# Performance work log

Hardware: AMD Instinct MI355X
Metric: run time of the kernel (lower is better)

Reference implementation:

```python
import jax, jax.numpy as jnp
import numpy as np

B = 1024          # batch
H = 512           # hidden_dim
T = 256           # seq_len
CD = 2            # coord_dim
LAT = 64 + 64 + 128  # total latent dim


def setup_inputs() -> dict:
    key = jax.random.key(0)
    ks = jax.random.split(key, 20)
    s = 0.05  # weight init scale
    rn = lambda k, shp: (jax.random.normal(k, shp, dtype=jnp.float32) * s)
    return {
        "z_primitive": jax.random.normal(ks[0], (B, 64), dtype=jnp.float32),
        "z_skill": jax.random.normal(ks[1], (B, 64), dtype=jnp.float32),
        "z_style": jax.random.normal(ks[2], (B, 128), dtype=jnp.float32),
        "W_proj": rn(ks[3], (2 * H, LAT)),
        "b_proj": jnp.zeros((2 * H,), jnp.float32),
        "Wih1": rn(ks[4], (4 * H, CD)),
        "Whh1": rn(ks[5], (4 * H, H)),
        "bih1": jnp.zeros((4 * H,), jnp.float32),
        "bhh1": jnp.zeros((4 * H,), jnp.float32),
        "Wih2": rn(ks[6], (4 * H, H)),
        "Whh2": rn(ks[7], (4 * H, H)),
        "bih2": jnp.zeros((4 * H,), jnp.float32),
        "bhh2": jnp.zeros((4 * H,), jnp.float32),
        "Wo1": rn(ks[8], (H // 2, H)),
        "bo1": jnp.zeros((H // 2,), jnp.float32),
        "Wo2": rn(ks[9], (CD, H // 2)),
        "bo2": jnp.zeros((CD,), jnp.float32),
    }


def _lstm_cell(x, h, c, Wih, Whh, bih, bhh):
    # PyTorch gate order: i, f, g, o
    gates = x @ Wih.T + h @ Whh.T + (bih + bhh)
    i, f, g, o = jnp.split(gates, 4, axis=1)
    c_new = jax.nn.sigmoid(f) * c + jax.nn.sigmoid(i) * jnp.tanh(g)
    h_new = jax.nn.sigmoid(o) * jnp.tanh(c_new)
    return h_new, c_new


def reference(z_primitive, z_skill, z_style, W_proj, b_proj,
              Wih1, Whh1, bih1, bhh1, Wih2, Whh2, bih2, bhh2,
              Wo1, bo1, Wo2, bo2):
    z = jnp.concatenate([z_primitive, z_skill, z_style], axis=1)  # [B, LAT]
    init = z @ W_proj.T + b_proj                                  # [B, 2H]
    h0 = init[:, :H]
    c0 = init[:, H:]
    x0 = jnp.zeros((z.shape[0], CD), init.dtype)

    def step(carry, _):
        x, h1, c1, h2, c2 = carry
        h1, c1 = _lstm_cell(x, h1, c1, Wih1, Whh1, bih1, bhh1)
        h2, c2 = _lstm_cell(h1, h2, c2, Wih2, Whh2, bih2, bhh2)
        # output MLP (Dropout inactive in eval)
        y = jax.nn.relu(h2 @ Wo1.T + bo1) @ Wo2.T + bo2  # [B, CD]
        return (y, h1, c1, h2, c2), y

    # h0/c0 repeated across both LSTM layers (repeat(2,1,1) in torch)
    _, ys = jax.lax.scan(step, (x0, h0, c0, h0, c0), None, length=T)
    return jnp.transpose(ys, (1, 0, 2))  # [B, T, CD]
```

## Files before the change

kernel.cpp:

```cpp
#include <hip/hip_runtime.h>
#include <math.h>

#define NB 1024
#define NH 512
#define NT 256
#define NCD 2

typedef unsigned short u16;
typedef __bf16 bf16x8 __attribute__((ext_vector_type(8)));
typedef float  f32x4  __attribute__((ext_vector_type(4)));

#define MFMA_BF16 __builtin_amdgcn_mfma_f32_16x16x32_bf16

__device__ __forceinline__ float sigf(float x) { return 1.0f / (1.0f + expf(-x)); }
__device__ __forceinline__ float b2f(u16 u) {
    union { unsigned i; float f; } v; v.i = ((unsigned)u) << 16; return v.f;
}
__device__ __forceinline__ u16 f2b(float f) {
    union { float f; unsigned i; } v; v.f = f;
    unsigned r = v.i + 0x7fffu + ((v.i >> 16) & 1u);
    return (u16)(r >> 16);
}

__device__ __forceinline__ void async_cp16(const void* gptr, void* lptr) {
    __builtin_amdgcn_global_load_lds(
        (const __attribute__((address_space(1))) unsigned int*)gptr,
        (__attribute__((address_space(3))) unsigned int*)lptr,
        16, 0, 0);
}

__global__ __launch_bounds__(256) void convert3(
    const float* __restrict__ a, const float* __restrict__ b,
    const float* __restrict__ c,
    u16* __restrict__ oa, u16* __restrict__ ob, u16* __restrict__ oc)
{
    const int i = blockIdx.x * 256 + threadIdx.x;
    oa[i] = f2b(a[i]); ob[i] = f2b(b[i]); oc[i] = f2b(c[i]);
}

__global__ __launch_bounds__(256) void bsum_k(
    const float* __restrict__ bi1, const float* __restrict__ bh1,
    const float* __restrict__ bi2, const float* __restrict__ bh2,
    float* __restrict__ o1, float* __restrict__ o2)
{
    const int i = blockIdx.x * 256 + threadIdx.x;
    o1[i] = bi1[i] + bh1[i];
    o2[i] = bi2[i] + bh2[i];
}

__global__ __launch_bounds__(256) void transpose_wo1(
    const float* __restrict__ Wo1, u16* __restrict__ Wo1T)
{
    const int idx = blockIdx.x * 256 + threadIdx.x;
    const int r = idx >> 9, k = idx & 511;
    Wo1T[k * 256 + r] = f2b(Wo1[idx]);
}

__global__ __launch_bounds__(256) void init_kernel(
    const float* __restrict__ zp, const float* __restrict__ zs,
    const float* __restrict__ zst, const float* __restrict__ Wp,
    const float* __restrict__ bp,
    u16* __restrict__ h1, float* __restrict__ c1,
    u16* __restrict__ h2, float* __restrict__ c2)
{
    __shared__ float z[4][256];
    const int tid = threadIdx.x;
    const int b0  = blockIdx.x * 4;
    for (int i = tid; i < 4 * 256; i += 256) {
        const int bb = i >> 8, k = i & 255;
        float v;
        if (k < 64)       v = zp [(b0 + bb) * 64  + k];
        else if (k < 128) v = zs [(b0 + bb) * 64  + (k - 64)];
        else              v = zst[(b0 + bb) * 128 + (k - 128)];
        z[bb][k] = v;
    }
    __syncthreads();
    for (int rt = 0; rt < 4; ++rt) {
        const int r = rt * 256 + tid;
        const float bias = bp[r];
        float a0 = bias, a1 = bias, a2 = bias, a3 = bias;
        for (int k = 0; k < 256; ++k) {
            const float w = Wp[r * 256 + k];
            a0 += z[0][k] * w; a1 += z[1][k] * w;
            a2 += z[2][k] * w; a3 += z[3][k] * w;
        }
        const float acc[4] = {a0, a1, a2, a3};
        for (int bb = 0; bb < 4; ++bb) {
            const int b = b0 + bb;
            if (r < NH) {
                h1[b * NH + r] = f2b(acc[bb]);
                h2[b * NH + r] = f2b(acc[bb]);
            } else {
                c1[b * NH + r - NH] = acc[bb];
                c2[b * NH + r - NH] = acc[bb];
            }
        }
    }
}

__global__ __launch_bounds__(512, 4) void lstm_mfma32(
    const u16* __restrict__ A0, const u16* __restrict__ W0,
    const u16* __restrict__ A1, const u16* __restrict__ W1,
    const float* __restrict__ bsum,
    const float* __restrict__ xin, const float* __restrict__ Wx,
    float* __restrict__ c, u16* __restrict__ hnext,
    const int npass)
{
    __shared__ __align__(16) char smem[61440];
    float* eg = (float*)smem;

    const int tid  = threadIdx.x;
    const int lane = tid & 63;
    const int wv   = tid >> 6;
    const int g    = wv & 3;
    const int mh   = wv >> 2;
    const int l15  = lane & 15;
    const int q    = lane >> 4;
    const int bx   = blockIdx.x;
    const int ut   = (bx & 7) * 2 + ((bx >> 3) & 1);
    const int grp  = bx >> 4;
    const int b0   = grp * 32;
    const int u0   = ut * 32;

    int goffW0, goffW1, goffA = 0;
    {
        const int c0 = (wv * 2) * 64 + lane;
        const int w0r = c0 >> 3;
        goffW0 = ((w0r >> 5) * NH + u0 + (w0r & 31)) * NH + (((c0 & 7) ^ (w0r & 7)) * 8);
        const int c1i = (wv * 2 + 1) * 64 + lane;
        const int w1r = c1i >> 3;
        goffW1 = ((w1r >> 5) * NH + u0 + (w1r & 31)) * NH + (((c1i & 7) ^ (w1r & 7)) * 8);
        if (wv < 4) {
            const int ca = wv * 64 + lane;
            const int ar = ca >> 3;
            goffA = (b0 + ar) * NH + (((ca & 7) ^ (ar & 7)) * 8);
        }
    }

    f32x4 acc[2];
    acc[0] = (f32x4){0.f, 0.f, 0.f, 0.f};
    acc[1] = (f32x4){0.f, 0.f, 0.f, 0.f};

    const int M = npass * 8;

    auto issue = [&](int m, int bi) {
        const u16* __restrict__ Ap = (m < 8) ? A0 : A1;
        const u16* __restrict__ Wp = (m < 8) ? W0 : W1;
        const int k0 = (m & 7) * 64;
        char* base = smem + bi * 20480;
        async_cp16((const void*)(Wp + goffW0 + k0),
                   (void*)(base + 4096 + (wv * 2) * 1024));
        async_cp16((const void*)(Wp + goffW1 + k0),
                   (void*)(base + 4096 + (wv * 2 + 1) * 1024));
        if (wv < 4)
            async_cp16((const void*)(Ap + goffA + k0),
                       (void*)(base + wv * 1024));
    };

    issue(0, 0);
    if (M > 1) issue(1, 1);
    int ci = 0;
    for (int m = 0; m < M; ++m) {
        if (m + 1 < M) {
            if (wv < 4) asm volatile("s_waitcnt vmcnt(3)" ::: "memory");
            else        asm volatile("s_waitcnt vmcnt(2)" ::: "memory");
        } else {
            asm volatile("s_waitcnt vmcnt(0)" ::: "memory");
        }
        __builtin_amdgcn_s_barrier();
        if (m + 2 < M) {
            int bi = ci + 2; if (bi >= 3) bi -= 3;
            issue(m + 2, bi);
        }
        const char* bA = smem + ci * 20480;
        const char* bW = bA + 4096;
#pragma unroll
        for (int khi = 0; khi < 2; ++khi) {
            bf16x8 bfr[2];
#pragma unroll
            for (int ni = 0; ni < 2; ++ni) {
                const int wrow = g * 32 + ni * 16 + l15;
                const int j = (khi * 4 + q) ^ (wrow & 7);
                bfr[ni] = *(const bf16x8*)(bW + wrow * 128 + j * 16);
            }
            const int row = mh * 16 + l15;
            const int j = (khi * 4 + q) ^ (row & 7);
            const bf16x8 av = *(const bf16x8*)(bA + row * 128 + j * 16);
            acc[0] = MFMA_BF16(av, bfr[0], acc[0], 0, 0, 0);
            acc[1] = MFMA_BF16(av, bfr[1], acc[1], 0, 0, 0);
        }
        ++ci; if (ci == 3) ci = 0;
    }

    __syncthreads();
#pragma unroll
    for (int ni = 0; ni < 2; ++ni)
#pragma unroll
        for (int r = 0; r < 4; ++r)
            eg[(g * 32 + mh * 16 + q * 4 + r) * 33 + ni * 16 + l15] = acc[ni][r];
    __syncthreads();

    const int u  = tid & 31;
    const int bq = tid >> 5;
    const int ug = u0 + u;
    float bs[4], wx0[4], wx1[4];
#pragma unroll
    for (int g4 = 0; g4 < 4; ++g4) bs[g4] = bsum[g4 * NH + ug];
    if (Wx) {
#pragma unroll
        for (int g4 = 0; g4 < 4; ++g4) {
            wx0[g4] = Wx[(g4 * NH + ug) * 2 + 0];
            wx1[g4] = Wx[(g4 * NH + ug) * 2 + 1];
        }
    }
#pragma unroll
    for (int jj = 0; jj < 2; ++jj) {
        const int bl = bq * 2 + jj;
        const int b  = b0 + bl;
        float gv[4];
#pragma unroll
        for (int g4 = 0; g4 < 4; ++g4) gv[g4] = eg[(g4 * 32 + bl) * 33 + u] + bs[g4];
        if (Wx) {
            const float x0 = xin[b * 2], x1 = xin[b * 2 + 1];
#pragma unroll
            for (int g4 = 0; g4 < 4; ++g4) gv[g4] += x0 * wx0[g4] + x1 * wx1[g4];
        }
        const float iv = sigf(gv[0]);
        const float fv = sigf(gv[1]);
        const float gg = tanhf(gv[2]);
        const float ov = sigf(gv[3]);
        const size_t idx = (size_t)b * NH + ug;
        const float cn = fv * c[idx] + iv * gg;
        c[idx] = cn;
        hnext[idx] = f2b(ov * tanhf(cn));
    }
}

__global__ __launch_bounds__(256) void out_kernel(
    const u16* __restrict__ h2, const u16* __restrict__ W1t,
    const float* __restrict__ bo1, const float* __restrict__ Wo2,
    const float* __restrict__ bo2, float* __restrict__ xbuf,
    float* __restrict__ out, const int t)
{
    __shared__ float hsh[2 * NH];
    __shared__ float red[4][4];
    const int tid = threadIdx.x;
    const int b0  = blockIdx.x * 2;
    for (int i = tid; i < 2 * NH; i += 256)
        hsh[i] = b2f(h2[(size_t)b0 * NH + i]);
    __syncthreads();

    const int n = tid;
    float a0 = 0.f, a1 = 0.f;
#pragma unroll 16
    for (int k = 0; k < NH; ++k) {
        const float w = b2f(W1t[k * 256 + n]);
        a0 += hsh[k] * w;
        a1 += hsh[NH + k] * w;
    }
    const float bn = bo1[n], w20 = Wo2[n], w21 = Wo2[256 + n];
    const float s0 = fmaxf(a0 + bn, 0.f), s1 = fmaxf(a1 + bn, 0.f);
    float p[4] = { s0 * w20, s0 * w21, s1 * w20, s1 * w21 };
#pragma unroll
    for (int off = 32; off > 0; off >>= 1)
#pragma unroll
        for (int r = 0; r < 4; ++r) p[r] += __shfl_down(p[r], off, 64);
    const int wave = tid >> 6, lane = tid & 63;
    if (lane == 0)
#pragma unroll
        for (int r = 0; r < 4; ++r) red[r][wave] = p[r];
    __syncthreads();
    if (tid < 4) {
        const int rp = tid >> 1, cc = tid & 1;
        const float v = red[tid][0] + red[tid][1] + red[tid][2] + red[tid][3]
                        + bo2[cc];
        const int b = b0 + rp;
        xbuf[b * NCD + cc] = v;
        out[(size_t)b * (NT * NCD) + t * NCD + cc] = v;
    }
}

extern "C" void kernel_launch(void* const* d_in, const int* in_sizes, int n_in,
                              void* d_out, int out_size, void* d_ws, size_t ws_size,
                              hipStream_t stream)
{
    const float* zp   = (const float*)d_in[0];
    const float* zsk  = (const float*)d_in[1];
    const float* zst  = (const float*)d_in[2];
    const float* Wp   = (const float*)d_in[3];
    const float* bp   = (const float*)d_in[4];
    const float* Wih1 = (const float*)d_in[5];
    const float* Whh1 = (const float*)d_in[6];
    const float* bih1 = (const float*)d_in[7];
    const float* bhh1 = (const float*)d_in[8];
    const float* Wih2 = (const float*)d_in[9];
    const float* Whh2 = (const float*)d_in[10];
    const float* bih2 = (const float*)d_in[11];
    const float* bhh2 = (const float*)d_in[12];
    const float* Wo1  = (const float*)d_in[13];
    const float* bo1  = (const float*)d_in[14];
    const float* Wo2  = (const float*)d_in[15];
    const float* bo2  = (const float*)d_in[16];

    const size_t BH = (size_t)NB * NH;
    u16*   h1a   = (u16*)d_ws;
    u16*   h1b   = h1a + BH;
    u16*   h2a   = h1b + BH;
    u16*   h2b   = h2a + BH;
    float* c1    = (float*)(h2b + BH);
    float* c2    = c1 + BH;
    float* xb    = c2 + BH;
    float* bs1   = xb + 4096;
    float* bs2   = bs1 + 2048;
    u16*   Wo1T  = (u16*)(bs2 + 2048);
    u16*   Whh1b = Wo1T + 131072;
    u16*   Wih2b = Whh1b + 1048576;
    u16*   Whh2b = Wih2b + 1048576;

    convert3<<<(2048 * 512) / 256, 256, 0, stream>>>(Whh1, Wih2, Whh2, Whh1b, Wih2b, Whh2b);
    transpose_wo1<<<(256 * 512) / 256, 256, 0, stream>>>(Wo1, Wo1T);
    bsum_k<<<2048 / 256, 256, 0, stream>>>(bih1, bhh1, bih2, bhh2, bs1, bs2);
    hipMemsetAsync(xb, 0, NB * NCD * sizeof(float), stream);
    init_kernel<<<NB / 4, 256, 0, stream>>>(zp, zsk, zst, Wp, bp, h1a, c1, h2a, c2);

    u16* h1c = h1a; u16* h1n = h1b;
    u16* h2c = h2a; u16* h2n = h2b;
    float* outp = (float*)d_out;
    for (int t = 0; t < NT; ++t) {
        lstm_mfma32<<<512, 512, 0, stream>>>(h1c, Whh1b, (const u16*)0, (const u16*)0,
                                             bs1, xb, Wih1, c1, h1n, 1);
        lstm_mfma32<<<512, 512, 0, stream>>>(h1n, Wih2b, h2c, Whh2b,
                                             bs2, (const float*)0, (const float*)0, c2, h2n, 2);
        out_kernel<<<512, 256, 0, stream>>>(h2n, Wo1T, bo1, Wo2, bo2, xb, outp, t);
        u16* tmp = h1c; h1c = h1n; h1n = tmp;
        tmp = h2c; h2c = h2n; h2n = tmp;
    }
}
```

Baseline: 8.472 ms.

## Fuse output MLP into layer-1 LSTM kernel with inter-block flag synchronization

```diff
diff --git a/kernel.cpp b/kernel.cpp
--- a/kernel.cpp
+++ b/kernel.cpp
@@ -95,6 +95,200 @@
                 c2[b * NH + r - NH] = acc[bb];
             }
         }
+    }
+}
+
+__global__ __launch_bounds__(512, 4) void fused_out_lstm1(
+    const u16* __restrict__ h2prev,
+    const u16* __restrict__ A0,
+    const u16* __restrict__ W0,
+    const float* __restrict__ bsum,
+    float* __restrict__ xb,
+    const float* __restrict__ Wx,
+    const u16* __restrict__ W1t, const float* __restrict__ bo1,
+    const float* __restrict__ Wo2, const float* __restrict__ bo2,
+    float* __restrict__ outp,
+    float* __restrict__ c, u16* __restrict__ hnext,
+    unsigned* __restrict__ flags,
+    const int t, const int do_lstm)
+{
+    __shared__ __align__(16) char smem[61440];
+    float* eg = (float*)smem;
+
+    const int tid  = threadIdx.x;
+    const int lane = tid & 63;
+    const int wv   = tid >> 6;
+    const int g    = wv & 3;
+    const int mh   = wv >> 2;
+    const int l15  = lane & 15;
+    const int q    = lane >> 4;
+    const int bx   = blockIdx.x;
+    const int ut   = (bx & 7) * 2 + ((bx >> 3) & 1);
+    const int grp  = bx >> 4;
+    const int b0   = grp * 32;
+    const int u0   = ut * 32;
+    const int r0   = grp * 32 + ut * 2;
+
+    int goffW0, goffW1, goffA = 0;
+    {
+        const int c0 = (wv * 2) * 64 + lane;
+        const int w0r = c0 >> 3;
+        goffW0 = ((w0r >> 5) * NH + u0 + (w0r & 31)) * NH + (((c0 & 7) ^ (w0r & 7)) * 8);
+        const int c1i = (wv * 2 + 1) * 64 + lane;
+        const int w1r = c1i >> 3;
+        goffW1 = ((w1r >> 5) * NH + u0 + (w1r & 31)) * NH + (((c1i & 7) ^ (w1r & 7)) * 8);
+        if (wv < 4) {
+            const int ca = wv * 64 + lane;
+            const int ar = ca >> 3;
+            goffA = (b0 + ar) * NH + (((ca & 7) ^ (ar & 7)) * 8);
+        }
+    }
+
+    auto issue = [&](int m, int bi) {
+        const int k0 = (m & 7) * 64;
+        char* base = smem + bi * 20480;
+        async_cp16((const void*)(W0 + goffW0 + k0),
+                   (void*)(base + 4096 + (wv * 2) * 1024));
+        async_cp16((const void*)(W0 + goffW1 + k0),
+                   (void*)(base + 4096 + (wv * 2 + 1) * 1024));
+        if (wv < 4)
+            async_cp16((const void*)(A0 + goffA + k0),
+                       (void*)(base + wv * 1024));
+    };
+
+    if (do_lstm) { issue(0, 0); issue(1, 1); }
+
+    if (h2prev) {
+        float* hsh = (float*)(smem + 40960);
+        float* red = (float*)(smem + 40960 + 4096);
+        for (int i = tid; i < 2 * NH; i += 512)
+            hsh[i] = b2f(h2prev[(size_t)(r0 + (i >> 9)) * NH + (i & 511)]);
+        asm volatile("s_waitcnt lgkmcnt(0)" ::: "memory");
+        __builtin_amdgcn_s_barrier();
+        const int n  = tid & 255;
+        const int hh = tid >> 8;
+        const float* hr = hsh + hh * NH;
+        float a = 0.f;
+#pragma unroll 16
+        for (int k = 0; k < NH; ++k)
+            a += hr[k] * b2f(W1t[k * 256 + n]);
+        const float s = fmaxf(a + bo1[n], 0.f);
+        float p0 = s * Wo2[n], p1 = s * Wo2[256 + n];
+#pragma unroll
+        for (int off = 32; off > 0; off >>= 1) {
+            p0 += __shfl_down(p0, off, 64);
+            p1 += __shfl_down(p1, off, 64);
+        }
+        if (lane == 0) { red[wv * 2] = p0; red[wv * 2 + 1] = p1; }
+        asm volatile("s_waitcnt lgkmcnt(0)" ::: "memory");
+        __builtin_amdgcn_s_barrier();
+        if (tid < 4) {
+            const int hh2 = tid >> 1, cc = tid & 1;
+            const int wb = hh2 * 4;
+            const float y = red[wb * 2 + cc] + red[(wb + 1) * 2 + cc]
+                          + red[(wb + 2) * 2 + cc] + red[(wb + 3) * 2 + cc]
+                          + bo2[cc];
+            const int b = r0 + hh2;
+            xb[b * NCD + cc] = y;
+            outp[(size_t)b * (NT * NCD) + (t - 1) * NCD + cc] = y;
+        }
+        if (wv == 0) {
+            __builtin_amdgcn_fence(__ATOMIC_RELEASE, "agent");
+            if (lane == 0 && do_lstm)
+                __hip_atomic_store(&flags[(grp * 16 + ut) * 16], (unsigned)t,
+                                   __ATOMIC_RELAXED, __HIP_MEMORY_SCOPE_AGENT);
+        }
+    }
+    if (!do_lstm) return;
+
+    f32x4 acc[2];
+    acc[0] = (f32x4){0.f, 0.f, 0.f, 0.f};
+    acc[1] = (f32x4){0.f, 0.f, 0.f, 0.f};
+    const int M = 8;
+    int ci = 0;
+    for (int m = 0; m < M; ++m) {
+        if (m + 1 < M) {
+            if (wv < 4) asm volatile("s_waitcnt vmcnt(3)" ::: "memory");
+            else        asm volatile("s_waitcnt vmcnt(2)" ::: "memory");
+        } else {
+            asm volatile("s_waitcnt vmcnt(0)" ::: "memory");
+        }
+        __builtin_amdgcn_s_barrier();
+        if (m + 2 < M) {
+            int bi = ci + 2; if (bi >= 3) bi -= 3;
+            issue(m + 2, bi);
+        }
+        const char* bA = smem + ci * 20480;
+        const char* bW = bA + 4096;
+#pragma unroll
+        for (int khi = 0; khi < 2; ++khi) {
+            bf16x8 bfr[2];
+#pragma unroll
+            for (int ni = 0; ni < 2; ++ni) {
+                const int wrow = g * 32 + ni * 16 + l15;
+                const int j = (khi * 4 + q) ^ (wrow & 7);
+                bfr[ni] = *(const bf16x8*)(bW + wrow * 128 + j * 16);
+            }
+            const int row = mh * 16 + l15;
+            const int j = (khi * 4 + q) ^ (row & 7);
+            const bf16x8 av = *(const bf16x8*)(bA + row * 128 + j * 16);
+            acc[0] = MFMA_BF16(av, bfr[0], acc[0], 0, 0, 0);
+            acc[1] = MFMA_BF16(av, bfr[1], acc[1], 0, 0, 0);
+        }
+        ++ci; if (ci == 3) ci = 0;
+    }
+
+    __syncthreads();
+#pragma unroll
+    for (int ni = 0; ni < 2; ++ni)
+#pragma unroll
+        for (int r = 0; r < 4; ++r)
+            eg[(g * 32 + mh * 16 + q * 4 + r) * 33 + ni * 16 + l15] = acc[ni][r];
+    __syncthreads();
+
+    if (t > 0) {
+        if (tid < 16) {
+            const unsigned tu = (unsigned)t;
+            while (__hip_atomic_load(&flags[(grp * 16 + tid) * 16],
+                                     __ATOMIC_RELAXED,
+                                     __HIP_MEMORY_SCOPE_AGENT) < tu)
+                __builtin_amdgcn_s_sleep(2);
+        }
+        __syncthreads();
+    }
+
+    const int u  = tid & 31;
+    const int bq = tid >> 5;
+    const int ug = u0 + u;
+    float bs[4], wx0[4], wx1[4];
+#pragma unroll
+    for (int g4 = 0; g4 < 4; ++g4) bs[g4] = bsum[g4 * NH + ug];
+#pragma unroll
+    for (int g4 = 0; g4 < 4; ++g4) {
+        wx0[g4] = Wx[(g4 * NH + ug) * 2 + 0];
+        wx1[g4] = Wx[(g4 * NH + ug) * 2 + 1];
+    }
+#pragma unroll
+    for (int jj = 0; jj < 2; ++jj) {
+        const int bl = bq * 2 + jj;
+        const int b  = b0 + bl;
+        float gv[4];
+#pragma unroll
+        for (int g4 = 0; g4 < 4; ++g4) gv[g4] = eg[(g4 * 32 + bl) * 33 + u] + bs[g4];
+        const float x0 = __hip_atomic_load(&xb[b * 2 + 0], __ATOMIC_RELAXED,
+                                           __HIP_MEMORY_SCOPE_AGENT);
+        const float x1 = __hip_atomic_load(&xb[b * 2 + 1], __ATOMIC_RELAXED,
+                                           __HIP_MEMORY_SCOPE_AGENT);
+#pragma unroll
+        for (int g4 = 0; g4 < 4; ++g4) gv[g4] += x0 * wx0[g4] + x1 * wx1[g4];
+        const float iv = sigf(gv[0]);
+        const float fv = sigf(gv[1]);
+        const float gg = tanhf(gv[2]);
+        const float ov = sigf(gv[3]);
+        const size_t idx = (size_t)b * NH + ug;
+        const float cn = fv * c[idx] + iv * gg;
+        c[idx] = cn;
+        hnext[idx] = f2b(ov * tanhf(cn));
     }
 }
 
@@ -233,50 +427,6 @@
         const float cn = fv * c[idx] + iv * gg;
         c[idx] = cn;
         hnext[idx] = f2b(ov * tanhf(cn));
-    }
-}
-
-__global__ __launch_bounds__(256) void out_kernel(
-    const u16* __restrict__ h2, const u16* __restrict__ W1t,
-    const float* __restrict__ bo1, const float* __restrict__ Wo2,
-    const float* __restrict__ bo2, float* __restrict__ xbuf,
-    float* __restrict__ out, const int t)
-{
-    __shared__ float hsh[2 * NH];
-    __shared__ float red[4][4];
-    const int tid = threadIdx.x;
-    const int b0  = blockIdx.x * 2;
-    for (int i = tid; i < 2 * NH; i += 256)
-        hsh[i] = b2f(h2[(size_t)b0 * NH + i]);
-    __syncthreads();
-
-    const int n = tid;
-    float a0 = 0.f, a1 = 0.f;
-#pragma unroll 16
-    for (int k = 0; k < NH; ++k) {
-        const float w = b2f(W1t[k * 256 + n]);
-        a0 += hsh[k] * w;
-        a1 += hsh[NH + k] * w;
-    }
-    const float bn = bo1[n], w20 = Wo2[n], w21 = Wo2[256 + n];
-    const float s0 = fmaxf(a0 + bn, 0.f), s1 = fmaxf(a1 + bn, 0.f);
-    float p[4] = { s0 * w20, s0 * w21, s1 * w20, s1 * w21 };
-#pragma unroll
-    for (int off = 32; off > 0; off >>= 1)
-#pragma unroll
-        for (int r = 0; r < 4; ++r) p[r] += __shfl_down(p[r], off, 64);
-    const int wave = tid >> 6, lane = tid & 63;
-    if (lane == 0)
-#pragma unroll
-        for (int r = 0; r < 4; ++r) red[r][wave] = p[r];
-    __syncthreads();
-    if (tid < 4) {
-        const int rp = tid >> 1, cc = tid & 1;
-        const float v = red[tid][0] + red[tid][1] + red[tid][2] + red[tid][3]
-                        + bo2[cc];
-        const int b = b0 + rp;
-        xbuf[b * NCD + cc] = v;
-        out[(size_t)b * (NT * NCD) + t * NCD + cc] = v;
     }
 }
 
@@ -316,23 +466,29 @@
     u16*   Whh1b = Wo1T + 131072;
     u16*   Wih2b = Whh1b + 1048576;
     u16*   Whh2b = Wih2b + 1048576;
+    unsigned* flags = (unsigned*)(Whh2b + 1048576);
 
     convert3<<<(2048 * 512) / 256, 256, 0, stream>>>(Whh1, Wih2, Whh2, Whh1b, Wih2b, Whh2b);
     transpose_wo1<<<(256 * 512) / 256, 256, 0, stream>>>(Wo1, Wo1T);
     bsum_k<<<2048 / 256, 256, 0, stream>>>(bih1, bhh1, bih2, bhh2, bs1, bs2);
     hipMemsetAsync(xb, 0, NB * NCD * sizeof(float), stream);
+    hipMemsetAsync(flags, 0, 32 * 16 * 16 * sizeof(unsigned), stream);
     init_kernel<<<NB / 4, 256, 0, stream>>>(zp, zsk, zst, Wp, bp, h1a, c1, h2a, c2);
 
     u16* h1c = h1a; u16* h1n = h1b;
     u16* h2c = h2a; u16* h2n = h2b;
     float* outp = (float*)d_out;
     for (int t = 0; t < NT; ++t) {
-        lstm_mfma32<<<512, 512, 0, stream>>>(h1c, Whh1b, (const u16*)0, (const u16*)0,
-                                             bs1, xb, Wih1, c1, h1n, 1);
+        fused_out_lstm1<<<512, 512, 0, stream>>>(
+            (t == 0) ? (const u16*)0 : h2c, h1c, Whh1b, bs1, xb, Wih1,
+            Wo1T, bo1, Wo2, bo2, outp, c1, h1n, flags, t, 1);
         lstm_mfma32<<<512, 512, 0, stream>>>(h1n, Wih2b, h2c, Whh2b,
-                                             bs2, (const float*)0, (const float*)0, c2, h2n, 2);
-        out_kernel<<<512, 256, 0, stream>>>(h2n, Wo1T, bo1, Wo2, bo2, xb, outp, t);
+                                             bs2, (const float*)0, (const float*)0,
+                                             c2, h2n, 2);
         u16* tmp = h1c; h1c = h1n; h1n = tmp;
         tmp = h2c; h2c = h2n; h2n = tmp;
     }
-}
+    fused_out_lstm1<<<512, 512, 0, stream>>>(
+        h2c, h1c, Whh1b, bs1, xb, Wih1,
+        Wo1T, bo1, Wo2, bo2, outp, c1, h1n, flags, NT, 0);
+}
```

Measured after the change: 11.12 ms. +31.2%, slower.
